# Performance work log

Measured on AMD Instinct MI355X. Metric: run time of the kernel, lower is better.

The kernel has to match this reference:

```python
import jax, jax.numpy as jnp
import numpy as np
from jax.scipy.special import logsumexp

B, N, K = 4, 2048, 20          # batch, points per cloud, knn neighbors
D_EMB, H = 512, 4              # embedding dim, attention heads
DH = D_EMB // H                # per-head dim (128)


def setup_inputs() -> dict:
    key = jax.random.key(0)
    ks = jax.random.split(key, 24)
    rn = lambda i, shape, s=0.05: jax.random.normal(ks[i], shape, jnp.float32) * s
    sc = lambda i, c: 1.0 + 0.1 * jax.random.normal(ks[i], (c,), jnp.float32)  # folded BN scale
    return {
        "src": jax.random.normal(ks[0], (B, 3, N), jnp.float32),
        "tgt": jax.random.normal(ks[1], (B, 3, N), jnp.float32),
        # GACLayer (shared for src/tgt): conv(6->64), conv(64->128), out conv(192->512); BN folded to scale/bias
        "g_w1": rn(2, (64, 6)),   "g_s1": sc(3, 64),  "g_b1": rn(4, (64,), 0.02),
        "g_w2": rn(5, (128, 64)), "g_s2": sc(6, 128), "g_b2": rn(7, (128,), 0.02),
        "g_wo": rn(8, (D_EMB, 192)), "g_so": sc(9, D_EMB), "g_bo": rn(10, (D_EMB,), 0.02),
        # MultiHeadedAttention: 3 projection 1x1 convs + merge (all with bias), mlp 1024->512 no bias
        "q_w": rn(11, (D_EMB, D_EMB)), "q_b": rn(12, (D_EMB,), 0.02),
        "k_w": rn(13, (D_EMB, D_EMB)), "k_b": rn(14, (D_EMB,), 0.02),
        "v_w": rn(15, (D_EMB, D_EMB)), "v_b": rn(16, (D_EMB,), 0.02),
        "m_w": rn(17, (D_EMB, D_EMB)), "m_b": rn(18, (D_EMB,), 0.02),
        "mlp_w": rn(19, (D_EMB, 2 * D_EMB)),
    }


def _forward(src, tgt, g_w1, g_s1, g_b1, g_w2, g_s2, g_b2, g_wo, g_so, g_bo,
             q_w, q_b, k_w, k_b, v_w, v_b, m_w, m_b, mlp_w):
    def knn_idx(x):                     # x: [B,3,N] -> [B,N,K] nearest-neighbor indices
        xx = jnp.sum(x * x, axis=1)                      # [B,N]
        inner = jnp.einsum('bdn,bdm->bnm', x, x)
        neg_d = 2.0 * inner - xx[:, :, None] - xx[:, None, :]   # negative sq dist
        return jax.lax.top_k(neg_d, K)[1]                # same as sort-descending[:k]

    def graph_feature(x):               # x: [B,D,N] -> [B,2D,N,K]
        idx = knn_idx(x)
        xt = x.transpose(0, 2, 1)                        # [B,N,D]
        feat = xt[jnp.arange(B)[:, None, None], idx]     # gather: [B,N,K,D]
        ctr = jnp.broadcast_to(xt[:, :, None, :], feat.shape)
        g = jnp.concatenate([feat - ctr, ctr], axis=-1)  # [B,N,K,2D]
        return g.transpose(0, 3, 1, 2)

    def conv_bn_relu2d(w, s, b, x):     # 1x1 conv2d + folded BN (eval) + relu
        y = jnp.einsum('oc,bcnk->bonk', w, x)
        return jax.nn.relu(y * s[:, None, None] + b[:, None, None])

    def attn_pool(h):                   # softmax over neighbors, weighted sum
        a = jax.nn.softmax(h, axis=-1)
        return jnp.sum(h * a, axis=-1)

    def gac(x):                         # GACLayer: [B,3,N] -> [B,512,N]
        g = graph_feature(x)            # [B,6,N,K]
        h1 = conv_bn_relu2d(g_w1, g_s1, g_b1, g)
        x1 = attn_pool(h1)              # [B,64,N]
        h2 = conv_bn_relu2d(g_w2, g_s2, g_b2, h1)
        x2 = attn_pool(h2)              # [B,128,N]
        o = jnp.einsum('oc,bcn->bon', g_wo, jnp.concatenate([x1, x2], axis=1))
        return jax.nn.relu(o * g_so[:, None] + g_bo[:, None])

    def proj(w, b, x):                  # 1x1 conv1d with bias
        return jnp.einsum('oi,bin->bon', w, x) + b[:, None]

    def mha(x, source):                 # note torch view splits channels as (dim, heads)
        q = proj(q_w, q_b, x).reshape(B, DH, H, -1)
        k_ = proj(k_w, k_b, source).reshape(B, DH, H, -1)
        v_ = proj(v_w, v_b, source).reshape(B, DH, H, -1)
        scores = jnp.einsum('bdhn,bdhm->bhnm', q, k_) / jnp.sqrt(jnp.float32(DH))
        prob = jax.nn.softmax(scores, axis=-1)
        msg = jnp.einsum('bhnm,bdhm->bdhn', prob, v_)
        return proj(m_w, m_b, msg.reshape(B, D_EMB, -1))

    def prop(x, source):                # AttentionalPropagation (mlp: 1024->512, no bias/relu)
        msg = mha(x, source)
        return jnp.einsum('oi,bin->bon', mlp_w, jnp.concatenate([x, msg], axis=1))

    def sinkhorn(scores, n_iters=5):    # log-domain Sinkhorn with dustbin row/col (zero pad)
        s = jnp.pad(scores, ((0, 0), (0, 1), (0, 1)))
        for _ in range(n_iters):
            s = jnp.concatenate(
                [s[:, :-1, :] - logsumexp(s[:, :-1, :], axis=2, keepdims=True), s[:, -1:, :]], axis=1)
            s = jnp.concatenate(
                [s[:, :, :-1] - logsumexp(s[:, :, :-1], axis=1, keepdims=True), s[:, :, -1:]], axis=2)
        return s[:, :-1, :-1]

    # embed + cross attentional GNN (shared layer, residual)
    d0, d1 = gac(src), gac(tgt)
    d0, d1 = d0 + prop(d0, d1), d1 + prop(d1, d0)

    dists = jnp.einsum('bdn,bdm->bnm', d0, d1) / jnp.sqrt(jnp.float32(D_EMB))
    perm = jnp.exp(sinkhorn(dists))
    perm_norm = perm / (jnp.sum(perm, axis=2, keepdims=True) + 1e-8)

    weighted_tgt = jnp.einsum('bdm,bnm->bdn', tgt, perm_norm)        # [B,3,N]
    weights = jnp.max(perm, axis=-1, keepdims=True)                  # [B,N,1]
    w_norm = (weights / (jnp.sum(weights, axis=1, keepdims=True) + 1e-8)).transpose(0, 2, 1)  # [B,1,N]
    src_c = jnp.sum(src * w_norm, axis=2, keepdims=True)             # [B,3,1]
    tgt_c = jnp.sum(weighted_tgt * w_norm, axis=2, keepdims=True)
    src_cent = src - src_c
    corr_cent = (weighted_tgt - tgt_c) * w_norm
    Hm = jnp.einsum('bdn,ben->bde', src_cent, corr_cent)             # [B,3,3]

    def solve(Hi):                      # Kabsch with reflection fix (torch.svd returns V, not V^T)
        u, s_, vt = jnp.linalg.svd(Hi)
        v = vt.T
        det = jnp.linalg.det(v @ u.T)
        diag = jnp.diag(jnp.concatenate([jnp.ones(2, Hi.dtype), det[None]]))
        return v @ diag @ u.T

    R = jax.vmap(solve)(Hm)
    t = (-jnp.einsum('bij,bjk->bik', R, src_c) + tgt_c).reshape(B, 3)
    return R, t, perm_norm


def reference(src, tgt, g_w1, g_s1, g_b1, g_w2, g_s2, g_b2, g_wo, g_so, g_bo,
              q_w, q_b, k_w, k_b, v_w, v_b, m_w, m_b, mlp_w):
    return _forward(src, tgt, g_w1, g_s1, g_b1, g_w2, g_s2, g_b2, g_wo, g_so, g_bo,
                    q_w, q_b, k_w, k_b, v_w, v_b, m_w, m_b, mlp_w)
```

## Files before the change

kernel.cpp:

```cpp
#include <hip/hip_runtime.h>
#include <math.h>

#define BATCH 4
#define NP    2048
#define KNNK  20
#define DEMB  512
#define NH    4
#define DHD   128

typedef __attribute__((ext_vector_type(8))) short bf16x8;
typedef __attribute__((ext_vector_type(4))) float f32x4;

__device__ __forceinline__ unsigned short f2b(float f) {
  unsigned u = __builtin_bit_cast(unsigned, f);
  u += 0x7FFF + ((u >> 16) & 1);
  return (unsigned short)(u >> 16);
}
__device__ __forceinline__ float b2f(unsigned short u) {
  unsigned v = ((unsigned)u) << 16;
  return __builtin_bit_cast(float, v);
}

__device__ __forceinline__ void gload_lds16(const void* g, void* l) {
  __builtin_amdgcn_global_load_lds(
      (const __attribute__((address_space(1))) unsigned int*)g,
      (__attribute__((address_space(3))) unsigned int*)l, 16, 0, 0);
}

__global__ void conv_all_kernel(const float* __restrict__ s0, const float* __restrict__ s1,
                                const float* __restrict__ s2, const float* __restrict__ s3,
                                const float* __restrict__ s4, const float* __restrict__ s5,
                                const float* __restrict__ s6,
                                unsigned short* __restrict__ d0, unsigned short* __restrict__ d1,
                                unsigned short* __restrict__ d2, unsigned short* __restrict__ d3,
                                unsigned short* __restrict__ d4, unsigned short* __restrict__ d5,
                                unsigned short* __restrict__ d6, float* __restrict__ vpot) {
  int i4 = (blockIdx.x * 256 + threadIdx.x) * 4;
  const float* src; unsigned short* dst; int off;
  if      (i4 < 262144)  { src = s0; dst = d0; off = i4; }
  else if (i4 < 524288)  { src = s1; dst = d1; off = i4 - 262144; }
  else if (i4 < 786432)  { src = s2; dst = d2; off = i4 - 524288; }
  else if (i4 < 1048576) { src = s3; dst = d3; off = i4 - 786432; }
  else if (i4 < 1572864) { src = s4; dst = d4; off = i4 - 1048576; }
  else if (i4 < 1581056) { src = s5; dst = d5; off = i4 - 1572864; }
  else if (i4 < 1679360) { src = s6; dst = d6; off = i4 - 1581056; }
  else if (i4 < 1687552) {
    off = i4 - 1679360;
    *(float4*)(vpot + off) = (float4){0.f, 0.f, 0.f, 0.f};
    return;
  } else return;
  float4 v = *(const float4*)(src + off);
  dst[off] = f2b(v.x); dst[off + 1] = f2b(v.y); dst[off + 2] = f2b(v.z); dst[off + 3] = f2b(v.w);
}

__global__ __launch_bounds__(256) void knn2_kernel(const float* __restrict__ x0,
                                                   const float* __restrict__ x1,
                                                   int* __restrict__ io0, int* __restrict__ io1) {
  __shared__ float xs0[NP], xs1[NP], xs2[NP];
  int which = blockIdx.x >> 11;
  int inner = blockIdx.x & 2047;
  const float* x = which ? x1 : x0;
  int* idx_out = which ? io1 : io0;
  int b = inner >> 9;
  int p0 = (inner & 511) * 4;
  int t = threadIdx.x, w = t >> 6, lane = t & 63;
  const float* xb = x + (size_t)b * 3 * NP;
  for (int m = t; m < NP; m += 256) {
    xs0[m] = xb[m]; xs1[m] = xb[NP + m]; xs2[m] = xb[2 * NP + m];
  }
  __syncthreads();
  int n = p0 + w;
  float c0 = xs0[n], c1 = xs1[n], c2 = xs2[n];
  float xxn = c0 * c0 + c1 * c1 + c2 * c2;
  float nd[32];
#pragma unroll
  for (int i = 0; i < 32; ++i) {
    int m = i * 64 + lane;
    float a0 = xs0[m], a1 = xs1[m], a2 = xs2[m];
    nd[i] = 2.f * (c0 * a0 + c1 * a1 + c2 * a2) - xxn - (a0 * a0 + a1 * a1 + a2 * a2);
  }
  unsigned sel = 0u;
  int* orow = idx_out + ((size_t)b * NP + n) * KNNK;
  for (int it = 0; it < KNNK; ++it) {
    float bv = -INFINITY; int bi = 0x7fffffff;
#pragma unroll
    for (int i = 0; i < 32; ++i) {
      float v = ((sel >> i) & 1u) ? -INFINITY : nd[i];
      if (v > bv) { bv = v; bi = i * 64 + lane; }
    }
#pragma unroll
    for (int s = 1; s < 64; s <<= 1) {
      float ov = __shfl_xor(bv, s);
      int oi = __shfl_xor(bi, s);
      if (ov > bv || (ov == bv && oi < bi)) { bv = ov; bi = oi; }
    }
    if (lane == 0) orow[it] = bi;
    if (lane == (bi & 63)) sel |= (1u << (bi >> 6));
  }
}

__global__ __launch_bounds__(256) void gac4_kernel(
    const float* __restrict__ x0, const float* __restrict__ x1,
    const int* __restrict__ io0, const int* __restrict__ io1,
    const float* __restrict__ w1, const float* __restrict__ s1, const float* __restrict__ b1,
    const unsigned short* __restrict__ w2b, const float* __restrict__ s2,
    const float* __restrict__ b2, unsigned short* __restrict__ xcg_all) {
  __shared__ __align__(16) float w1p[448];
  __shared__ float s1s[64], b1s[64];
  __shared__ float g[4][6][20];
  __shared__ __align__(16) float h1f[4][20][65];
  __shared__ __align__(16) unsigned short h1b[4 * 2048];
  int which = blockIdx.x >> 11;
  int inner = blockIdx.x & 2047;
  const float* x = which ? x1 : x0;
  const int* idx = which ? io1 : io0;
  unsigned short* xcg = xcg_all + (size_t)which * BATCH * NP * 192;
  int t = threadIdx.x, w = t >> 6, lane = t & 63;
  int lr = lane & 15, lg = lane >> 4;
  int b = inner >> 9;
  int n0g = (inner & 511) * 4;
  int pbase = b * NP + n0g;
  const float* xb = x + (size_t)b * 3 * NP;

  for (int i = t; i < 384; i += 256) { int o = i / 6, c = i % 6; w1p[o * 7 + c] = w1[i]; }
  if (t < 64) { s1s[t] = s1[t]; b1s[t] = b1[t]; }
  if (t < 80) {
    int p = t / 20, k = t % 20;
    int n = n0g + p;
    int j = idx[((size_t)b * NP + n) * KNNK + k];
    float c0 = xb[n], c1 = xb[NP + n], c2 = xb[2 * NP + n];
    g[p][0][k] = xb[j] - c0; g[p][1][k] = xb[NP + j] - c1; g[p][2][k] = xb[2 * NP + j] - c2;
    g[p][3][k] = c0; g[p][4][k] = c1; g[p][5][k] = c2;
  }
  for (int i = t; i < 4 * 12 * 32; i += 256) {
    int p = i / 384, rem = i % 384;
    ((unsigned*)h1b)[p * 1024 + (20 + rem / 32) * 32 + (rem & 31)] = 0u;
  }
  __syncthreads();

#pragma unroll
  for (int pass = 0; pass < 20; ++pass) {
    int item = pass * 256 + t;
    int o = item & 63, kp = item >> 6;
    int k = kp % 20, p = kp / 20;
    float y = 0.f;
#pragma unroll
    for (int c = 0; c < 6; ++c) y += w1p[o * 7 + c] * g[p][c][k];
    y = fmaxf(y * s1s[o] + b1s[o], 0.f);
    h1f[p][k][o] = y;
    h1b[p * 2048 + k * 64 + (((o >> 3) ^ (k & 7)) << 3) + (o & 7)] = f2b(y);
  }
  __syncthreads();

  {
    int p = w, o = lane;
    float mx = -INFINITY;
#pragma unroll
    for (int k = 0; k < 20; ++k) mx = fmaxf(mx, h1f[p][k][o]);
    float se = 0.f, sh = 0.f;
#pragma unroll
    for (int k = 0; k < 20; ++k) {
      float h = h1f[p][k][o];
      float e = __expf(h - mx);
      se += e; sh += h * e;
    }
    xcg[(size_t)(pbase + p) * 192 + o] = f2b(sh / se);
  }

  bf16x8 bfrag[2][2];
#pragma unroll
  for (int ks = 0; ks < 2; ++ks)
#pragma unroll
    for (int nt = 0; nt < 2; ++nt) {
      int kcol = nt * 16 + lr;
      int oc = ks * 4 + lg;
      bfrag[ks][nt] = *(const bf16x8*)&h1b[w * 2048 + kcol * 64 + ((oc ^ (kcol & 7)) << 3)];
    }
  f32x4 acc[8][2];
#pragma unroll
  for (int i = 0; i < 8; ++i) { acc[i][0] = (f32x4){0,0,0,0}; acc[i][1] = (f32x4){0,0,0,0}; }
#pragma unroll
  for (int i = 0; i < 8; ++i)
#pragma unroll
    for (int ks = 0; ks < 2; ++ks) {
      bf16x8 a = *(const bf16x8*)(w2b + (i * 16 + lr) * 64 + ks * 32 + lg * 8);
      acc[i][0] = __builtin_amdgcn_mfma_f32_16x16x32_bf16(a, bfrag[ks][0], acc[i][0], 0, 0, 0);
      acc[i][1] = __builtin_amdgcn_mfma_f32_16x16x32_bf16(a, bfrag[ks][1], acc[i][1], 0, 0, 0);
    }
  int pt = pbase + w;
#pragma unroll
  for (int i = 0; i < 8; ++i) {
    float x2o[4];
#pragma unroll
    for (int r = 0; r < 4; ++r) {
      int o = i * 16 + lg * 4 + r;
      float sv = s2[o], bv = b2[o];
      float v0 = fmaxf(acc[i][0][r] * sv + bv, 0.f);
      float v1 = fmaxf(acc[i][1][r] * sv + bv, 0.f);
      float vm = (lr < 4) ? fmaxf(v0, v1) : v0;
#pragma unroll
      for (int s = 1; s < 16; s <<= 1) vm = fmaxf(vm, __shfl_xor(vm, s));
      float e0 = __expf(v0 - vm);
      float e1 = (lr < 4) ? __expf(v1 - vm) : 0.f;
      float se = e0 + e1, sh = v0 * e0 + v1 * e1;
#pragma unroll
      for (int s = 1; s < 16; s <<= 1) { se += __shfl_xor(se, s); sh += __shfl_xor(sh, s); }
      x2o[r] = sh / se;
    }
    if (lr == 0) {
      ushort4 pk;
      pk.x = f2b(x2o[0]); pk.y = f2b(x2o[1]); pk.z = f2b(x2o[2]); pk.w = f2b(x2o[3]);
      *(ushort4*)&xcg[(size_t)pt * 192 + 64 + i * 16 + lg * 4] = pk;
    }
  }
}

__global__ __launch_bounds__(256, 2) void gacproj_kernel(
    const unsigned short* __restrict__ wob, const float* __restrict__ so,
    const float* __restrict__ bo, const unsigned short* __restrict__ xcg,
    unsigned short* __restrict__ Y0, unsigned short* __restrict__ Y1) {
  __shared__ __align__(16) unsigned short Al[128 * 64];
  __shared__ __align__(16) unsigned short Bl[128 * 64];
  int n0 = blockIdx.x * 128, o0 = blockIdx.y * 128;
  unsigned short* Yt = (n0 < BATCH * NP) ? Y0 : Y1;
  int nbase = n0 & (BATCH * NP - 1);
  int tid = threadIdx.x, w = tid >> 6, lane = tid & 63;
  int lr = lane & 15, lg = lane >> 4;
  int wa = w >> 1, wb = w & 1;
  f32x4 acc[4][4];
#pragma unroll
  for (int i = 0; i < 4; ++i)
#pragma unroll
    for (int j = 0; j < 4; ++j) acc[i][j] = (f32x4){0.f, 0.f, 0.f, 0.f};

  for (int k0 = 0; k0 < 192; k0 += 64) {
    __syncthreads();
#pragma unroll
    for (int u = 0; u < 4; ++u) {
      int C = u * 256 + tid;
      int row = C >> 3, j = C & 7;
      int js = j ^ (row & 7);
      gload_lds16(wob + (size_t)(o0 + row) * 192 + k0 + js * 8, Al + (u * 256 + w * 64) * 8);
      gload_lds16(xcg + (size_t)(n0 + row) * 192 + k0 + js * 8, Bl + (u * 256 + w * 64) * 8);
    }
    asm volatile("s_waitcnt vmcnt(0)" ::: "memory");
    __syncthreads();
#pragma unroll
    for (int kk = 0; kk < 2; ++kk) {
      bf16x8 af[4], bfr[4];
#pragma unroll
      for (int i = 0; i < 4; ++i) {
        int rowa = wa * 64 + i * 16 + lr;
        int ca = (kk * 4 + lg) ^ (rowa & 7);
        af[i] = *(const bf16x8*)(Al + rowa * 64 + ca * 8);
        int rowb = wb * 64 + i * 16 + lr;
        int cb = (kk * 4 + lg) ^ (rowb & 7);
        bfr[i] = *(const bf16x8*)(Bl + rowb * 64 + cb * 8);
      }
#pragma unroll
      for (int i = 0; i < 4; ++i)
#pragma unroll
        for (int j = 0; j < 4; ++j)
          acc[i][j] = __builtin_amdgcn_mfma_f32_16x16x32_bf16(af[i], bfr[j], acc[i][j], 0, 0, 0);
    }
  }
#pragma unroll
  for (int i = 0; i < 4; ++i) {
#pragma unroll
    for (int j = 0; j < 4; ++j) {
      int obase = o0 + wa * 64 + i * 16 + lg * 4;
      int n = nbase + wb * 64 + j * 16 + lr;
      ushort4 pk;
      pk.x = f2b(fmaxf(acc[i][j][0] * so[obase] + bo[obase], 0.f));
      pk.y = f2b(fmaxf(acc[i][j][1] * so[obase + 1] + bo[obase + 1], 0.f));
      pk.z = f2b(fmaxf(acc[i][j][2] * so[obase + 2] + bo[obase + 2], 0.f));
      pk.w = f2b(fmaxf(acc[i][j][3] * so[obase + 3] + bo[obase + 3], 0.f));
      *(ushort4*)&Yt[(size_t)n * DEMB + obase] = pk;
    }
  }
}

__global__ __launch_bounds__(256, 2) void qkv_kernel(
    const unsigned short* __restrict__ qw, const unsigned short* __restrict__ kw,
    const unsigned short* __restrict__ vw, const float* __restrict__ qbias,
    const float* __restrict__ kbias, const float* __restrict__ vbias,
    const unsigned short* __restrict__ d0t, const unsigned short* __restrict__ d1t,
    unsigned short* __restrict__ Q0, unsigned short* __restrict__ K0,
    unsigned short* __restrict__ V0, unsigned short* __restrict__ Q1,
    unsigned short* __restrict__ K1, unsigned short* __restrict__ V1) {
  __shared__ __align__(16) unsigned short Al[128 * 64];
  __shared__ __align__(16) unsigned short Bl[128 * 64];
  int z = blockIdx.z;
  int b = z & 3, which = z >> 2;
  int proj = which % 3, side = which / 3;
  const unsigned short* Wb = (proj == 0) ? qw : (proj == 1) ? kw : vw;
  const float* bias = (proj == 0) ? qbias : (proj == 1) ? kbias : vbias;
  const unsigned short* Bt = side ? d1t : d0t;
  unsigned short* Y = (which == 0) ? Q0 : (which == 1) ? K0 : (which == 2) ? V0
                    : (which == 3) ? Q1 : (which == 4) ? K1 : V1;
  float pscale = (proj == 0) ? 0.08838834764831845f : 1.f;
  int n0 = blockIdx.x * 128, o0 = blockIdx.y * 128;
  int tid = threadIdx.x, w = tid >> 6, lane = tid & 63;
  int lr = lane & 15, lg = lane >> 4;
  int wa = w >> 1, wb = w & 1;
  f32x4 acc[4][4];
#pragma unroll
  for (int i = 0; i < 4; ++i)
#pragma unroll
    for (int j = 0; j < 4; ++j) acc[i][j] = (f32x4){0.f, 0.f, 0.f, 0.f};

  for (int k0 = 0; k0 < DEMB; k0 += 64) {
    __syncthreads();
#pragma unroll
    for (int u = 0; u < 4; ++u) {
      int C = u * 256 + tid;
      int row = C >> 3, j = C & 7;
      int js = j ^ (row & 7);
      gload_lds16(Wb + (size_t)(o0 + row) * DEMB + k0 + js * 8, Al + (u * 256 + w * 64) * 8);
      gload_lds16(Bt + ((size_t)b * NP + n0 + row) * 512 + k0 + js * 8,
                  Bl + (u * 256 + w * 64) * 8);
    }
    asm volatile("s_waitcnt vmcnt(0)" ::: "memory");
    __syncthreads();
#pragma unroll
    for (int kk = 0; kk < 2; ++kk) {
      bf16x8 af[4], bfr[4];
#pragma unroll
      for (int i = 0; i < 4; ++i) {
        int rowa = wa * 64 + i * 16 + lr;
        int ca = (kk * 4 + lg) ^ (rowa & 7);
        af[i] = *(const bf16x8*)(Al + rowa * 64 + ca * 8);
        int rowb = wb * 64 + i * 16 + lr;
        int cb = (kk * 4 + lg) ^ (rowb & 7);
        bfr[i] = *(const bf16x8*)(Bl + rowb * 64 + cb * 8);
      }
#pragma unroll
      for (int i = 0; i < 4; ++i)
#pragma unroll
        for (int j = 0; j < 4; ++j)
          acc[i][j] = __builtin_amdgcn_mfma_f32_16x16x32_bf16(af[i], bfr[j], acc[i][j], 0, 0, 0);
    }
  }
#pragma unroll
  for (int i = 0; i < 4; ++i) {
#pragma unroll
    for (int j = 0; j < 4; ++j) {
#pragma unroll
      for (int r = 0; r < 4; ++r) {
        int o = o0 + wa * 64 + i * 16 + lg * 4 + r;
        int n = n0 + wb * 64 + j * 16 + lr;
        float v = (acc[i][j][r] + bias[o]) * pscale;
        int h = o & 3, dh = o >> 2;
        if (proj < 2) {
          Y[(((size_t)b * NH + h) * NP + n) * DHD + dh] = f2b(v);
        } else {
          Y[(((size_t)b * NH + h) * DHD + dh) * NP + n] = f2b(v);
        }
      }
    }
  }
}

template <int MODE, int KD>
__global__ __launch_bounds__(256, 2) void proj_mfma_kernel(
    const unsigned short* __restrict__ Wb, const float* __restrict__ bias,
    const unsigned short* __restrict__ Bt0, const unsigned short* __restrict__ Bt1,
    const unsigned short* __restrict__ Bt2_0, const unsigned short* __restrict__ Bt2_1,
    const unsigned short* __restrict__ D0, const unsigned short* __restrict__ D1,
    unsigned short* __restrict__ Y0, unsigned short* __restrict__ Y1) {
  __shared__ __align__(16) unsigned short Al[128 * 64];
  __shared__ __align__(16) unsigned short Bl[128 * 64];
  int z = blockIdx.z;
  int b = z & 3, side = z >> 2;
  const unsigned short* Bt = side ? Bt1 : Bt0;
  const unsigned short* Bt2 = side ? Bt2_1 : Bt2_0;
  const unsigned short* Dres = side ? D1 : D0;
  unsigned short* Y = side ? Y1 : Y0;
  int n0 = blockIdx.x * 128, o0 = blockIdx.y * 128;
  int tid = threadIdx.x, w = tid >> 6, lane = tid & 63;
  int lr = lane & 15, lg = lane >> 4;
  int wa = w >> 1, wb = w & 1;
  f32x4 acc[4][4];
#pragma unroll
  for (int i = 0; i < 4; ++i)
#pragma unroll
    for (int j = 0; j < 4; ++j) acc[i][j] = (f32x4){0.f, 0.f, 0.f, 0.f};

  for (int k0 = 0; k0 < KD; k0 += 64) {
    __syncthreads();
    const unsigned short* srcB; int kc;
    if (MODE == 4) { srcB = (k0 < 512) ? Bt : Bt2; kc = k0 & 511; }
    else { srcB = Bt; kc = k0; }
#pragma unroll
    for (int u = 0; u < 4; ++u) {
      int C = u * 256 + tid;
      int row = C >> 3, j = C & 7;
      int js = j ^ (row & 7);
      gload_lds16(Wb + (size_t)(o0 + row) * KD + k0 + js * 8, Al + (u * 256 + w * 64) * 8);
      gload_lds16(srcB + ((size_t)b * NP + n0 + row) * 512 + kc + js * 8,
                  Bl + (u * 256 + w * 64) * 8);
    }
    asm volatile("s_waitcnt vmcnt(0)" ::: "memory");
    __syncthreads();
#pragma unroll
    for (int kk = 0; kk < 2; ++kk) {
      bf16x8 af[4], bfr[4];
#pragma unroll
      for (int i = 0; i < 4; ++i) {
        int rowa = wa * 64 + i * 16 + lr;
        int ca = (kk * 4 + lg) ^ (rowa & 7);
        af[i] = *(const bf16x8*)(Al + rowa * 64 + ca * 8);
        int rowb = wb * 64 + i * 16 + lr;
        int cb = (kk * 4 + lg) ^ (rowb & 7);
        bfr[i] = *(const bf16x8*)(Bl + rowb * 64 + cb * 8);
      }
#pragma unroll
      for (int i = 0; i < 4; ++i)
#pragma unroll
        for (int j = 0; j < 4; ++j)
          acc[i][j] = __builtin_amdgcn_mfma_f32_16x16x32_bf16(af[i], bfr[j], acc[i][j], 0, 0, 0);
    }
  }
#pragma unroll
  for (int i = 0; i < 4; ++i) {
#pragma unroll
    for (int j = 0; j < 4; ++j) {
#pragma unroll
      for (int r = 0; r < 4; ++r) {
        int o = o0 + wa * 64 + i * 16 + lg * 4 + r;
        int n = n0 + wb * 64 + j * 16 + lr;
        float v = acc[i][j][r];
        if (MODE == 3) {
          v += bias[o];
        } else {
          v += b2f(Dres[((size_t)b * NP + n) * DEMB + o]);
        }
        Y[((size_t)b * NP + n) * DEMB + o] = f2b(v);
      }
    }
  }
}

__global__ __launch_bounds__(256, 2) void attn_mfma_kernel(
    const unsigned short* __restrict__ Q0, const unsigned short* __restrict__ K0,
    const unsigned short* __restrict__ V0, const unsigned short* __restrict__ Q1,
    const unsigned short* __restrict__ K1, const unsigned short* __restrict__ V1,
    unsigned short* __restrict__ att0, unsigned short* __restrict__ att1) {
  __shared__ __align__(16) unsigned short Klds[2][8192];
  __shared__ __align__(16) unsigned short Vlds[2][8192];
  __shared__ __align__(16) float Pws[4][544];

  int which = blockIdx.x >> 9;
  int blk = blockIdx.x & 511;
  const unsigned short* Qb = which ? Q1 : Q0;
  const unsigned short* Kb = which ? K0 : K1;
  const unsigned short* Vb = which ? V0 : V1;
  unsigned short* att = which ? att1 : att0;

  int bh = blk >> 5, qt = blk & 31;
  int tid = threadIdx.x;
  int w = tid >> 6, lane = tid & 63;
  int lr = lane & 15, lg = lane >> 4;
  int q0 = qt * 64 + w * 16;

  const unsigned short* Qrow = Qb + ((size_t)bh * NP + q0 + lr) * DHD + lg * 8;
  bf16x8 qf[4];
#pragma unroll
  for (int ds = 0; ds < 4; ++ds) qf[ds] = *(const bf16x8*)(Qrow + ds * 32);

  const unsigned short* Kg = Kb + (size_t)bh * NP * DHD;
  const unsigned short* Vg = Vb + (size_t)bh * DHD * NP;
  unsigned short* Pl = (unsigned short*)&Pws[w][0];

  f32x4 o[8];
#pragma unroll
  for (int ds = 0; ds < 8; ++ds) o[ds] = (f32x4){0.f, 0.f, 0.f, 0.f};
  float mrun[4] = {-INFINITY, -INFINITY, -INFINITY, -INFINITY};
  float lrun[4] = {0.f, 0.f, 0.f, 0.f};

#pragma unroll
  for (int u = 0; u < 4; ++u) {
    int C = (w * 4 + u) * 64 + lane;
    int key = C >> 4, jl = C & 15, j = jl ^ (key & 15);
    gload_lds16(Kg + (size_t)key * DHD + j * 8, &Klds[0][(w * 4 + u) * 512]);
    int d = C >> 3, jv = (C & 7) ^ (d & 7);
    gload_lds16(Vg + (size_t)d * NP + jv * 8, &Vlds[0][(w * 4 + u) * 512]);
  }
  asm volatile("s_waitcnt vmcnt(0)" ::: "memory");
  __syncthreads();

  for (int tIdx = 0; tIdx < 32; ++tIdx) {
    int cur = tIdx & 1;
    if (tIdx < 31) {
      int kv0 = (tIdx + 1) * 64;
#pragma unroll
      for (int u = 0; u < 4; ++u) {
        int C = (w * 4 + u) * 64 + lane;
        int key = C >> 4, jl = C & 15, j = jl ^ (key & 15);
        gload_lds16(Kg + (size_t)(kv0 + key) * DHD + j * 8, &Klds[cur ^ 1][(w * 4 + u) * 512]);
        int d = C >> 3, jv = (C & 7) ^ (d & 7);
        gload_lds16(Vg + (size_t)d * NP + kv0 + jv * 8, &Vlds[cur ^ 1][(w * 4 + u) * 512]);
      }
    }
    f32x4 s[4];
#pragma unroll
    for (int ks = 0; ks < 4; ++ks) {
      s[ks] = (f32x4){0.f, 0.f, 0.f, 0.f};
      int key = ks * 16 + lr;
#pragma unroll
      for (int dstep = 0; dstep < 4; ++dstep) {
        int dbyte = (lg * 16 + dstep * 64) ^ ((key & 15) << 4);
        bf16x8 kb = *(const bf16x8*)(&Klds[cur][0] + key * 128 + (dbyte >> 1));
        s[ks] = __builtin_amdgcn_mfma_f32_16x16x32_bf16(qf[dstep], kb, s[ks], 0, 0, 0);
      }
    }
    float tmax[4];
#pragma unroll
    for (int r = 0; r < 4; ++r) {
      float m = fmaxf(fmaxf(s[0][r], s[1][r]), fmaxf(s[2][r], s[3][r]));
#pragma unroll
      for (int msk = 1; msk < 16; msk <<= 1) m = fmaxf(m, __shfl_xor(m, msk));
      tmax[r] = m;
    }
    int need = 0;
#pragma unroll
    for (int r = 0; r < 4; ++r) need |= (tmax[r] > mrun[r]) ? 1 : 0;
    float fac[4] = {1.f, 1.f, 1.f, 1.f};
    if (__any(need)) {
#pragma unroll
      for (int r = 0; r < 4; ++r) {
        float mnew = fmaxf(mrun[r], tmax[r]);
        fac[r] = __expf(mrun[r] - mnew);
        mrun[r] = mnew;
      }
#pragma unroll
      for (int ds = 0; ds < 8; ++ds)
#pragma unroll
        for (int r = 0; r < 4; ++r) o[ds][r] *= fac[r];
    }
    float ps[4] = {0.f, 0.f, 0.f, 0.f};
#pragma unroll
    for (int ks = 0; ks < 4; ++ks) {
      int k = ks * 16 + lr;
#pragma unroll
      for (int r = 0; r < 4; ++r) {
        float p = __expf(s[ks][r] - mrun[r]);
        ps[r] += p;
        int q = lg * 4 + r;
        int kbyte = (k * 2) ^ ((q & 7) << 4);
        Pl[q * 64 + (kbyte >> 1)] = f2b(p);
      }
    }
#pragma unroll
    for (int r = 0; r < 4; ++r) {
#pragma unroll
      for (int msk = 1; msk < 16; msk <<= 1) ps[r] += __shfl_xor(ps[r], msk);
      lrun[r] = lrun[r] * fac[r] + ps[r];
    }
#pragma unroll
    for (int ks2 = 0; ks2 < 2; ++ks2) {
      int kbyte = ((lg * 8 + ks2 * 32) * 2) ^ ((lr & 7) << 4);
      bf16x8 pa = *(const bf16x8*)(Pl + lr * 64 + (kbyte >> 1));
#pragma unroll
      for (int ds = 0; ds < 8; ++ds) {
        int d = ds * 16 + lr;
        int keybyte = ((lg * 8 + ks2 * 32) * 2) ^ ((d & 7) << 4);
        bf16x8 vb = *(const bf16x8*)(&Vlds[cur][0] + d * 64 + (keybyte >> 1));
        o[ds] = __builtin_amdgcn_mfma_f32_16x16x32_bf16(pa, vb, o[ds], 0, 0, 0);
      }
    }
    asm volatile("s_waitcnt vmcnt(0)" ::: "memory");
    __syncthreads();
  }

  float linv[4];
#pragma unroll
  for (int r = 0; r < 4; ++r) linv[r] = 1.f / lrun[r];
  float* ost = &Pws[w][0];
  int b = bh >> 2, h = bh & 3;
  unsigned short* outb = att + ((size_t)b * NP + q0) * DEMB;
#pragma unroll
  for (int c = 0; c < 4; ++c) {
#pragma unroll
    for (int half = 0; half < 2; ++half) {
      int ds = 2 * c + half;
#pragma unroll
      for (int r = 0; r < 4; ++r)
        ost[(lg * 4 + r) * 33 + half * 16 + lr] = o[ds][r] * linv[r];
    }
    __syncthreads();
#pragma unroll
    for (int it = 0; it < 8; ++it) {
      int q = lr, dl = it * 4 + lg;
      int d = c * 32 + dl;
      outb[(size_t)q * DEMB + d * 4 + h] = f2b(ost[q * 33 + dl]);
    }
    __syncthreads();
  }
}

__global__ __launch_bounds__(256, 2) void dists_mfma_kernel(
    const unsigned short* __restrict__ At, const unsigned short* __restrict__ Bt,
    unsigned short* __restrict__ S) {
  __shared__ __align__(16) unsigned short Sh[2][8192];
  int b = blockIdx.z;
  int n0 = blockIdx.y * 128, m0 = blockIdx.x * 128;
  int tid = threadIdx.x, w = tid >> 6, lane = tid & 63;
  int lr = lane & 15, lg = lane >> 4;
  int wn = w >> 1, wm = w & 1;
  const unsigned short* Ab = At + ((size_t)b * NP + n0) * DEMB;
  const unsigned short* Bb = Bt + ((size_t)b * NP + m0) * DEMB;
  f32x4 acc[4][4];
#pragma unroll
  for (int i = 0; i < 4; ++i)
#pragma unroll
    for (int j = 0; j < 4; ++j) acc[i][j] = (f32x4){0.f, 0.f, 0.f, 0.f};

  for (int k0 = 0; k0 < DEMB; k0 += 64) {
    __syncthreads();
#pragma unroll
    for (int u = 0; u < 4; ++u) {
      int C = u * 256 + tid;
      int row = C >> 3, j = C & 7;
      int js = j ^ (row & 7);
      gload_lds16(Ab + (size_t)row * DEMB + k0 + js * 8, &Sh[0][(u * 256 + w * 64) * 8]);
      gload_lds16(Bb + (size_t)row * DEMB + k0 + js * 8, &Sh[1][(u * 256 + w * 64) * 8]);
    }
    asm volatile("s_waitcnt vmcnt(0)" ::: "memory");
    __syncthreads();
#pragma unroll
    for (int kk = 0; kk < 2; ++kk) {
      bf16x8 af[4], bfr[4];
#pragma unroll
      for (int i = 0; i < 4; ++i) {
        int rowa = wn * 64 + i * 16 + lr;
        int ca = (kk * 4 + lg) ^ (rowa & 7);
        af[i] = *(const bf16x8*)(&Sh[0][0] + rowa * 64 + ca * 8);
        int rowb = wm * 64 + i * 16 + lr;
        int cb = (kk * 4 + lg) ^ (rowb & 7);
        bfr[i] = *(const bf16x8*)(&Sh[1][0] + rowb * 64 + cb * 8);
      }
#pragma unroll
      for (int i = 0; i < 4; ++i)
#pragma unroll
        for (int j = 0; j < 4; ++j)
          acc[i][j] = __builtin_amdgcn_mfma_f32_16x16x32_bf16(af[i], bfr[j], acc[i][j], 0, 0, 0);
    }
  }
  const float scale = 0.04419417382415922f;
  __syncthreads();
  unsigned short* Cs = &Sh[0][0];
#pragma unroll
  for (int i = 0; i < 4; ++i)
#pragma unroll
    for (int j = 0; j < 4; ++j)
#pragma unroll
      for (int r = 0; r < 4; ++r) {
        int nl = wn * 64 + i * 16 + lg * 4 + r;
        int ml = wm * 64 + j * 16 + lr;
        Cs[nl * 128 + ml] = f2b(acc[i][j][r] * scale);
      }
  __syncthreads();
  unsigned short* Sb = S + (size_t)b * NP * NP;
#pragma unroll
  for (int it = 0; it < 8; ++it) {
    int chunk = it * 256 + tid;
    int rowl = chunk >> 4, c8 = (chunk & 15) * 8;
    *(bf16x8*)(Sb + (size_t)(n0 + rowl) * NP + m0 + c8) = *(const bf16x8*)(Cs + rowl * 128 + c8);
  }
}

__global__ __launch_bounds__(256) void sink_u_kernel(const unsigned short* __restrict__ S,
                                                     const float* __restrict__ v,
                                                     float* __restrict__ u) {
  int t = threadIdx.x, w = t >> 6, lane = t & 63;
  int rowid = blockIdx.x * 4 + w;
  int b = rowid >> 11, i = rowid & 2047;
  const unsigned short* row = S + ((size_t)b * NP + i) * NP;
  const float* vb = v + (size_t)b * NP;
  float m = -INFINITY, s = 0.f;
#pragma unroll
  for (int c = 0; c < 4; ++c) {
    int off = c * 512 + lane * 8;
    bf16x8 x8 = *(const bf16x8*)(row + off);
    float4 va = *(const float4*)(vb + off);
    float4 vc = *(const float4*)(vb + off + 4);
    float xs[8];
    xs[0] = b2f(x8[0]) + va.x; xs[1] = b2f(x8[1]) + va.y;
    xs[2] = b2f(x8[2]) + va.z; xs[3] = b2f(x8[3]) + va.w;
    xs[4] = b2f(x8[4]) + vc.x; xs[5] = b2f(x8[5]) + vc.y;
    xs[6] = b2f(x8[6]) + vc.z; xs[7] = b2f(x8[7]) + vc.w;
    float mc = fmaxf(fmaxf(fmaxf(xs[0], xs[1]), fmaxf(xs[2], xs[3])),
                     fmaxf(fmaxf(xs[4], xs[5]), fmaxf(xs[6], xs[7])));
    float sc = 0.f;
#pragma unroll
    for (int e = 0; e < 8; ++e) sc += __expf(xs[e] - mc);
    float M = fmaxf(m, mc);
    s = s * __expf(m - M) + sc * __expf(mc - M);
    m = M;
  }
#pragma unroll
  for (int st = 1; st < 64; st <<= 1) {
    float m2 = __shfl_xor(m, st), s2 = __shfl_xor(s, st);
    float M = fmaxf(m, m2);
    s = s * __expf(m - M) + s2 * __expf(m2 - M);
    m = M;
  }
  if (lane == 0) {
    float M = fmaxf(m, 0.f);
    float ss = s * __expf(m - M) + __expf(-M);
    u[(size_t)b * NP + i] = -(M + logf(ss));
  }
}

__global__ void sink_c1_kernel(const unsigned short* __restrict__ S, const float* __restrict__ u,
                               float* __restrict__ colM, float* __restrict__ colS) {
  int ctile = blockIdx.x, part = blockIdx.y, b = blockIdx.z;
  int t = threadIdx.x, ry = t >> 6, cx = t & 63;
  int c0 = ctile * 128 + cx * 2;
  int rbase = part * 256 + ry * 64;
  const unsigned short* Sb = S + (size_t)b * NP * NP;
  const float* ub = u + (size_t)b * NP;
  float m0 = -INFINITY, s0 = 0.f, m1 = -INFINITY, s1 = 0.f;
  for (int r8 = 0; r8 < 64; r8 += 8) {
    float x0[8], x1[8];
#pragma unroll
    for (int k = 0; k < 8; ++k) {
      int r = rbase + r8 + k;
      unsigned pk = *(const unsigned*)(Sb + (size_t)r * NP + c0);
      float uu = ub[r];
      x0[k] = b2f((unsigned short)pk) + uu;
      x1[k] = b2f((unsigned short)(pk >> 16)) + uu;
    }
    float mc0 = x0[0], mc1 = x1[0];
#pragma unroll
    for (int k = 1; k < 8; ++k) { mc0 = fmaxf(mc0, x0[k]); mc1 = fmaxf(mc1, x1[k]); }
    float sc0 = 0.f, sc1 = 0.f;
#pragma unroll
    for (int k = 0; k < 8; ++k) { sc0 += __expf(x0[k] - mc0); sc1 += __expf(x1[k] - mc1); }
    float M0 = fmaxf(m0, mc0);
    s0 = s0 * __expf(m0 - M0) + sc0 * __expf(mc0 - M0); m0 = M0;
    float M1 = fmaxf(m1, mc1);
    s1 = s1 * __expf(m1 - M1) + sc1 * __expf(mc1 - M1); m1 = M1;
  }
  __shared__ float pm[4][128], ps[4][128];
  pm[ry][cx * 2] = m0; pm[ry][cx * 2 + 1] = m1;
  ps[ry][cx * 2] = s0; ps[ry][cx * 2 + 1] = s1;
  __syncthreads();
  if (t < 128) {
    float m = pm[0][t], s = ps[0][t];
    for (int k = 1; k < 4; ++k) {
      float m2 = pm[k][t], s2 = ps[k][t];
      float M = fmaxf(m, m2);
      s = s * __expf(m - M) + s2 * __expf(m2 - M);
      m = M;
    }
    size_t oo = ((size_t)b * NP + ctile * 128 + t) * 8 + part;
    colM[oo] = m; colS[oo] = s;
  }
}

__global__ void sink_c2_kernel(const float* __restrict__ colM, const float* __restrict__ colS,
                               float* __restrict__ v) {
  int i = blockIdx.x * 256 + threadIdx.x;
  if (i >= BATCH * NP) return;
  float m = -INFINITY, s = 0.f;
  for (int p = 0; p < 8; ++p) {
    float m2 = colM[(size_t)i * 8 + p], s2 = colS[(size_t)i * 8 + p];
    float M = fmaxf(m, m2);
    s = s * __expf(m - M) + s2 * __expf(m2 - M);
    m = M;
  }
  float M = fmaxf(m, 0.f);
  s = s * __expf(m - M) + __expf(-M);
  v[i] = -(M + logf(s));
}

__global__ void perm_kernel(const unsigned short* __restrict__ S, const float* __restrict__ u,
                            const float* __restrict__ v, const float* __restrict__ tgt,
                            float* __restrict__ outp, float* __restrict__ weights,
                            float* __restrict__ wt) {
  int b = blockIdx.x / NP, n = blockIdx.x % NP, t = threadIdx.x;
  const unsigned short* row = S + ((size_t)b * NP + n) * NP;
  const float* vb = v + (size_t)b * NP;
  float ui = u[(size_t)b * NP + n];
  __shared__ float reds[256], redm[256];
  int c0 = t * 8;
  bf16x8 x8 = *(const bf16x8*)(row + c0);
  float4 va = *(const float4*)(vb + c0);
  float4 vc = *(const float4*)(vb + c0 + 4);
  float ev[8];
  ev[0] = __expf(b2f(x8[0]) + ui + va.x); ev[1] = __expf(b2f(x8[1]) + ui + va.y);
  ev[2] = __expf(b2f(x8[2]) + ui + va.z); ev[3] = __expf(b2f(x8[3]) + ui + va.w);
  ev[4] = __expf(b2f(x8[4]) + ui + vc.x); ev[5] = __expf(b2f(x8[5]) + ui + vc.y);
  ev[6] = __expf(b2f(x8[6]) + ui + vc.z); ev[7] = __expf(b2f(x8[7]) + ui + vc.w);
  float lsum = 0.f, lm = -INFINITY;
#pragma unroll
  for (int e = 0; e < 8; ++e) { lsum += ev[e]; lm = fmaxf(lm, ev[e]); }
  reds[t] = lsum; redm[t] = lm;
  __syncthreads();
  for (int st = 128; st > 0; st >>= 1) {
    if (t < st) { reds[t] += reds[t + st]; redm[t] = fmaxf(redm[t], redm[t + st]); }
    __syncthreads();
  }
  float inv = 1.f / (reds[0] + 1e-8f);
  float mx = redm[0];
  __syncthreads();
  const float* tb = tgt + (size_t)b * 3 * NP;
  float* op = outp + ((size_t)b * NP + n) * NP;
  float pn[8];
#pragma unroll
  for (int e = 0; e < 8; ++e) pn[e] = ev[e] * inv;
  float4 o0 = {pn[0], pn[1], pn[2], pn[3]};
  float4 o1 = {pn[4], pn[5], pn[6], pn[7]};
  *(float4*)(op + c0) = o0;
  *(float4*)(op + c0 + 4) = o1;
  float av[3];
#pragma unroll
  for (int d = 0; d < 3; ++d) {
    const float* td = tb + d * NP;
    float4 ta = *(const float4*)(td + c0);
    float4 tc = *(const float4*)(td + c0 + 4);
    av[d] = pn[0] * ta.x + pn[1] * ta.y + pn[2] * ta.z + pn[3] * ta.w +
            pn[4] * tc.x + pn[5] * tc.y + pn[6] * tc.z + pn[7] * tc.w;
  }
  for (int d = 0; d < 3; ++d) {
    reds[t] = av[d];
    __syncthreads();
    for (int st = 128; st > 0; st >>= 1) { if (t < st) reds[t] += reds[t + st]; __syncthreads(); }
    if (t == 0) wt[((size_t)b * 3 + d) * NP + n] = reds[0];
    __syncthreads();
  }
  if (t == 0) weights[(size_t)b * NP + n] = mx;
}

__global__ void wsum_kernel(const float* __restrict__ weights, float* __restrict__ wsum) {
  int b = blockIdx.x, t = threadIdx.x;
  __shared__ float red[256];
  float s = 0.f;
  for (int n = t; n < NP; n += 256) s += weights[(size_t)b * NP + n];
  red[t] = s;
  __syncthreads();
  for (int st = 128; st > 0; st >>= 1) { if (t < st) red[t] += red[t + st]; __syncthreads(); }
  if (t == 0) wsum[b] = red[0];
}

__global__ void cent_hm_kernel(const float* __restrict__ src, const float* __restrict__ wt,
                               const float* __restrict__ weights, const float* __restrict__ wsum,
                               float* __restrict__ cent, float* __restrict__ Hm) {
  int b = blockIdx.x, t = threadIdx.x;
  __shared__ float red[256];
  __shared__ float cc[6];
  float inv = 1.f / (wsum[b] + 1e-8f);
  const float* sb = src + (size_t)b * 3 * NP;
  const float* wb = wt + (size_t)b * 3 * NP;
  const float* ww = weights + (size_t)b * NP;
  float acc[6] = {};
  for (int n = t; n < NP; n += 256) {
    float w = ww[n] * inv;
    acc[0] += sb[n] * w;        acc[1] += sb[NP + n] * w;  acc[2] += sb[2 * NP + n] * w;
    acc[3] += wb[n] * w;        acc[4] += wb[NP + n] * w;  acc[5] += wb[2 * NP + n] * w;
  }
  for (int i = 0; i < 6; ++i) {
    red[t] = acc[i];
    __syncthreads();
    for (int st = 128; st > 0; st >>= 1) { if (t < st) red[t] += red[t + st]; __syncthreads(); }
    if (t == 0) cc[i] = red[0];
    __syncthreads();
  }
  float h[9] = {};
  for (int n = t; n < NP; n += 256) {
    float w = ww[n] * inv;
    float s0 = sb[n] - cc[0], s1 = sb[NP + n] - cc[1], s2 = sb[2 * NP + n] - cc[2];
    float d0 = (wb[n] - cc[3]) * w, d1 = (wb[NP + n] - cc[4]) * w, d2 = (wb[2 * NP + n] - cc[5]) * w;
    h[0] += s0 * d0; h[1] += s0 * d1; h[2] += s0 * d2;
    h[3] += s1 * d0; h[4] += s1 * d1; h[5] += s1 * d2;
    h[6] += s2 * d0; h[7] += s2 * d1; h[8] += s2 * d2;
  }
  for (int i = 0; i < 9; ++i) {
    red[t] = h[i];
    __syncthreads();
    for (int st = 128; st > 0; st >>= 1) { if (t < st) red[t] += red[t + st]; __syncthreads(); }
    if (t == 0) Hm[b * 9 + i] = red[0];
    __syncthreads();
  }
  if (t == 0) for (int i = 0; i < 6; ++i) cent[b * 6 + i] = cc[i];
}

__device__ double det3d(const double M[3][3]) {
  return M[0][0] * (M[1][1] * M[2][2] - M[1][2] * M[2][1])
       - M[0][1] * (M[1][0] * M[2][2] - M[1][2] * M[2][0])
       + M[0][2] * (M[1][0] * M[2][1] - M[1][1] * M[2][0]);
}

#define JROT(p, q)                                                              \
  do {                                                                          \
    double apq = S[p][q];                                                       \
    if (fabs(apq) > 1e-60) {                                                    \
      double tau = (S[q][q] - S[p][p]) / (2.0 * apq);                           \
      double tt = (tau >= 0.0) ? 1.0 / (tau + sqrt(1.0 + tau * tau))            \
                               : 1.0 / (tau - sqrt(1.0 + tau * tau));           \
      double cr = 1.0 / sqrt(1.0 + tt * tt), sr = tt * cr;                      \
      _Pragma("unroll") for (int k = 0; k < 3; ++k) {                           \
        double skp = S[k][p], skq = S[k][q];                                    \
        S[k][p] = cr * skp - sr * skq;  S[k][q] = sr * skp + cr * skq;          \
      }                                                                         \
      _Pragma("unroll") for (int k = 0; k < 3; ++k) {                           \
        double spk = S[p][k], sqk = S[q][k];                                    \
        S[p][k] = cr * spk - sr * sqk;  S[q][k] = sr * spk + cr * sqk;          \
      }                                                                         \
      _Pragma("unroll") for (int k = 0; k < 3; ++k) {                           \
        double vkp = V[k][p], vkq = V[k][q];                                    \
        V[k][p] = cr * vkp - sr * vkq;  V[k][q] = sr * vkp + cr * vkq;          \
      }                                                                         \
    }                                                                           \
  } while (0)

#define CSWAPCOL(i, j, ei, ej)                                                  \
  if (ei < ej) {                                                                \
    double tt_ = ei; ei = ej; ej = tt_;                                         \
    _Pragma("unroll") for (int r = 0; r < 3; ++r) {                             \
      double tv = V[r][i]; V[r][i] = V[r][j]; V[r][j] = tv;                     \
    }                                                                           \
  }

__global__ void solve_kernel(const float* __restrict__ Hm, const float* __restrict__ cent,
                             float* __restrict__ out) {
  int b = threadIdx.x;
  if (b >= BATCH) return;
  double A[3][3];
#pragma unroll
  for (int r = 0; r < 3; ++r)
#pragma unroll
    for (int c = 0; c < 3; ++c) A[r][c] = (double)Hm[b * 9 + r * 3 + c];
  double S[3][3];
#pragma unroll
  for (int i = 0; i < 3; ++i)
#pragma unroll
    for (int j = 0; j < 3; ++j) {
      double acc = 0.0;
#pragma unroll
      for (int k = 0; k < 3; ++k) acc += A[k][i] * A[k][j];
      S[i][j] = acc;
    }
  double V[3][3] = {{1, 0, 0}, {0, 1, 0}, {0, 0, 1}};
  for (int sweep = 0; sweep < 12; ++sweep) {
    JROT(0, 1); JROT(0, 2); JROT(1, 2);
  }
  double e0 = S[0][0], e1 = S[1][1], e2 = S[2][2];
  CSWAPCOL(0, 1, e0, e1);
  CSWAPCOL(0, 2, e0, e2);
  CSWAPCOL(1, 2, e1, e2);
  double Us[3][3];
#pragma unroll
  for (int i = 0; i < 3; ++i) {
    double v0 = V[0][i], v1 = V[1][i], v2 = V[2][i];
    double u0 = A[0][0] * v0 + A[0][1] * v1 + A[0][2] * v2;
    double u1 = A[1][0] * v0 + A[1][1] * v1 + A[1][2] * v2;
    double u2 = A[2][0] * v0 + A[2][1] * v1 + A[2][2] * v2;
    double nrm = sqrt(u0 * u0 + u1 * u1 + u2 * u2);
    if (nrm > 1e-30) { u0 /= nrm; u1 /= nrm; u2 /= nrm; }
    else if (i == 2) {
      u0 = Us[1][0] * Us[2][1] - Us[2][0] * Us[1][1];
      u1 = Us[2][0] * Us[0][1] - Us[0][0] * Us[2][1];
      u2 = Us[0][0] * Us[1][1] - Us[1][0] * Us[0][1];
      double nn = sqrt(u0 * u0 + u1 * u1 + u2 * u2);
      if (nn > 1e-30) { u0 /= nn; u1 /= nn; u2 /= nn; }
    }
    Us[0][i] = u0; Us[1][i] = u1; Us[2][i] = u2;
  }
  double d = det3d(V) * det3d(Us);
  double R[3][3];
#pragma unroll
  for (int i = 0; i < 3; ++i)
#pragma unroll
    for (int j = 0; j < 3; ++j)
      R[i][j] = V[i][0] * Us[j][0] + V[i][1] * Us[j][1] + d * V[i][2] * Us[j][2];
  double sc[3] = {(double)cent[b * 6 + 0], (double)cent[b * 6 + 1], (double)cent[b * 6 + 2]};
  double tc[3] = {(double)cent[b * 6 + 3], (double)cent[b * 6 + 4], (double)cent[b * 6 + 5]};
#pragma unroll
  for (int r = 0; r < 3; ++r)
#pragma unroll
    for (int c = 0; c < 3; ++c) out[b * 9 + r * 3 + c] = (float)R[r][c];
#pragma unroll
  for (int i = 0; i < 3; ++i) {
    double tv = tc[i] - (R[i][0] * sc[0] + R[i][1] * sc[1] + R[i][2] * sc[2]);
    out[36 + b * 3 + i] = (float)tv;
  }
}

extern "C" void kernel_launch(void* const* d_in, const int* in_sizes, int n_in,
                              void* d_out, int out_size, void* d_ws, size_t ws_size,
                              hipStream_t stream) {
  const float* src  = (const float*)d_in[0];
  const float* tgt  = (const float*)d_in[1];
  const float* g_w1 = (const float*)d_in[2];
  const float* g_s1 = (const float*)d_in[3];
  const float* g_b1 = (const float*)d_in[4];
  const float* g_w2 = (const float*)d_in[5];
  const float* g_s2 = (const float*)d_in[6];
  const float* g_b2 = (const float*)d_in[7];
  const float* g_wo = (const float*)d_in[8];
  const float* g_so = (const float*)d_in[9];
  const float* g_bo = (const float*)d_in[10];
  const float* q_w  = (const float*)d_in[11];
  const float* q_b  = (const float*)d_in[12];
  const float* k_w  = (const float*)d_in[13];
  const float* k_b  = (const float*)d_in[14];
  const float* v_w  = (const float*)d_in[15];
  const float* v_b  = (const float*)d_in[16];
  const float* m_w  = (const float*)d_in[17];
  const float* m_b  = (const float*)d_in[18];
  const float* mlp_w = (const float*)d_in[19];
  float* out = (float*)d_out;
  float* ws = (float*)d_ws;

  const size_t SLOT = 4194304;
  unsigned short* d0t  = (unsigned short*)(ws + 0 * SLOT);
  unsigned short* d1t  = (unsigned short*)(ws + 1 * SLOT);
  unsigned short* Q0   = (unsigned short*)(ws + 2 * SLOT);
  unsigned short* K0   = (unsigned short*)(ws + 3 * SLOT);
  unsigned short* V0   = (unsigned short*)(ws + 4 * SLOT);
  unsigned short* Q1   = (unsigned short*)(ws + 5 * SLOT);
  unsigned short* K1   = (unsigned short*)(ws + 6 * SLOT);
  unsigned short* V1   = (unsigned short*)(ws + 7 * SLOT);
  unsigned short* att0t = (unsigned short*)(ws + 8 * SLOT);
  unsigned short* att1t = (unsigned short*)(ws + 9 * SLOT);
  unsigned short* mp0t = Q0;
  unsigned short* mp1t = Q1;
  unsigned short* d0nt = att0t;
  unsigned short* d1nt = att1t;
  unsigned short* base3  = (unsigned short*)(ws + 3 * SLOT);
  unsigned short* q_wb   = base3 + 4456448;
  unsigned short* k_wb   = q_wb + 262144;
  unsigned short* v_wb   = k_wb + 262144;
  unsigned short* m_wb   = v_wb + 262144;
  unsigned short* mlp_wb = m_wb + 262144;
  unsigned short* w2b    = mlp_wb + 524288;
  unsigned short* wob    = w2b + 8192;
  unsigned short* xcg    = att0t;
  unsigned short* SbU = (unsigned short*)ws;
  int*   idx0 = (int*)(ws + 10 * SLOT);
  int*   idx1 = idx0 + BATCH * NP * KNNK;
  float* colM = ws + 10 * SLOT + 327680;
  float* colS = colM + BATCH * NP * 8;
  float* weights = colS + BATCH * NP * 8;
  float* wsum = weights + BATCH * NP;
  float* wtg  = wsum + BATCH;
  float* cent = wtg + BATCH * 3 * NP;
  float* Hmb  = cent + BATCH * 6;
  float* upot = Hmb + BATCH * 9;
  float* vpot = upot + BATCH * NP;

  conv_all_kernel<<<1648, 256, 0, stream>>>(q_w, k_w, v_w, m_w, mlp_w, g_w2, g_wo,
                                            q_wb, k_wb, v_wb, m_wb, mlp_wb, w2b, wob, vpot);
  knn2_kernel<<<2 * BATCH * NP / 4, 256, 0, stream>>>(src, tgt, idx0, idx1);
  gac4_kernel<<<2 * BATCH * NP / 4, 256, 0, stream>>>(src, tgt, idx0, idx1, g_w1, g_s1, g_b1,
                                                      w2b, g_s2, g_b2, xcg);
  dim3 gg(2 * BATCH * NP / 128, DEMB / 128);
  gacproj_kernel<<<gg, 256, 0, stream>>>(wob, g_so, g_bo, xcg, d0t, d1t);
  dim3 gqkv(NP / 128, DEMB / 128, 24);
  qkv_kernel<<<gqkv, 256, 0, stream>>>(q_wb, k_wb, v_wb, q_b, k_b, v_b, d0t, d1t,
                                       Q0, K0, V0, Q1, K1, V1);
  attn_mfma_kernel<<<2 * 16 * 32, 256, 0, stream>>>(Q0, K0, V0, Q1, K1, V1, att0t, att1t);
  dim3 gq8(NP / 128, DEMB / 128, 8);
  proj_mfma_kernel<3, 512><<<gq8, 256, 0, stream>>>(m_wb, m_b, att0t, att1t, nullptr, nullptr,
                                                    nullptr, nullptr, mp0t, mp1t);
  proj_mfma_kernel<4, 1024><<<gq8, 256, 0, stream>>>(mlp_wb, nullptr, d0t, d1t, mp0t, mp1t,
                                                     d0t, d1t, d0nt, d1nt);
  dists_mfma_kernel<<<dim3(NP / 128, NP / 128, BATCH), 256, 0, stream>>>(d0nt, d1nt, SbU);
  for (int it = 0; it < 5; ++it) {
    sink_u_kernel<<<BATCH * NP / 4, 256, 0, stream>>>(SbU, vpot, upot);
    sink_c1_kernel<<<dim3(NP / 128, 8, BATCH), 256, 0, stream>>>(SbU, upot, colM, colS);
    sink_c2_kernel<<<(BATCH * NP + 255) / 256, 256, 0, stream>>>(colM, colS, vpot);
  }
  perm_kernel<<<BATCH * NP, 256, 0, stream>>>(SbU, upot, vpot, tgt, out + 48, weights, wtg);
  wsum_kernel<<<BATCH, 256, 0, stream>>>(weights, wsum);
  cent_hm_kernel<<<BATCH, 256, 0, stream>>>(src, wtg, weights, wsum, cent, Hmb);
  solve_kernel<<<1, 64, 0, stream>>>(Hmb, cent, out);
}
```

Measured before the change: 680.9 us.

## Load V directly into registers in attention, drop V LDS staging, raise occupancy

The attention kernel stops staging V tiles through LDS and instead loads each wave's V fragments straight from global memory into registers at the start of every KV step. This frees half the LDS, which allows the launch bound to go from 2 to 3 blocks per CU. The change also raises wave priority around the MFMA sections and removes the block barriers in the per-wave output staging epilogue. The risks are that the V global loads are no longer prefetched a tile ahead, so their latency is exposed in each iteration, 16 extra vector registers per thread add pressure, and several waves now fetch the same V rows from global memory.

Measured after the change: 996.9 us. 1.46x slower.

```diff
diff --git a/kernel.cpp b/kernel.cpp
--- a/kernel.cpp
+++ b/kernel.cpp
@@ -441,13 +441,12 @@
   }
 }
 
-__global__ __launch_bounds__(256, 2) void attn_mfma_kernel(
+__global__ __launch_bounds__(256, 3) void attn_mfma_kernel(
     const unsigned short* __restrict__ Q0, const unsigned short* __restrict__ K0,
     const unsigned short* __restrict__ V0, const unsigned short* __restrict__ Q1,
     const unsigned short* __restrict__ K1, const unsigned short* __restrict__ V1,
     unsigned short* __restrict__ att0, unsigned short* __restrict__ att1) {
   __shared__ __align__(16) unsigned short Klds[2][8192];
-  __shared__ __align__(16) unsigned short Vlds[2][8192];
   __shared__ __align__(16) float Pws[4][544];
 
   int which = blockIdx.x >> 9;
@@ -483,25 +482,30 @@
     int C = (w * 4 + u) * 64 + lane;
     int key = C >> 4, jl = C & 15, j = jl ^ (key & 15);
     gload_lds16(Kg + (size_t)key * DHD + j * 8, &Klds[0][(w * 4 + u) * 512]);
-    int d = C >> 3, jv = (C & 7) ^ (d & 7);
-    gload_lds16(Vg + (size_t)d * NP + jv * 8, &Vlds[0][(w * 4 + u) * 512]);
   }
   asm volatile("s_waitcnt vmcnt(0)" ::: "memory");
   __syncthreads();
 
   for (int tIdx = 0; tIdx < 32; ++tIdx) {
     int cur = tIdx & 1;
+    int kv0 = tIdx * 64;
+    bf16x8 vreg[16];
+#pragma unroll
+    for (int ks2 = 0; ks2 < 2; ++ks2)
+#pragma unroll
+      for (int ds = 0; ds < 8; ++ds)
+        vreg[ks2 * 8 + ds] =
+            *(const bf16x8*)(Vg + (size_t)(ds * 16 + lr) * NP + kv0 + ks2 * 32 + lg * 8);
     if (tIdx < 31) {
-      int kv0 = (tIdx + 1) * 64;
+      int kn = kv0 + 64;
 #pragma unroll
       for (int u = 0; u < 4; ++u) {
         int C = (w * 4 + u) * 64 + lane;
         int key = C >> 4, jl = C & 15, j = jl ^ (key & 15);
-        gload_lds16(Kg + (size_t)(kv0 + key) * DHD + j * 8, &Klds[cur ^ 1][(w * 4 + u) * 512]);
-        int d = C >> 3, jv = (C & 7) ^ (d & 7);
-        gload_lds16(Vg + (size_t)d * NP + kv0 + jv * 8, &Vlds[cur ^ 1][(w * 4 + u) * 512]);
+        gload_lds16(Kg + (size_t)(kn + key) * DHD + j * 8, &Klds[cur ^ 1][(w * 4 + u) * 512]);
       }
     }
+    __builtin_amdgcn_s_setprio(1);
     f32x4 s[4];
 #pragma unroll
     for (int ks = 0; ks < 4; ++ks) {
@@ -514,6 +518,7 @@
         s[ks] = __builtin_amdgcn_mfma_f32_16x16x32_bf16(qf[dstep], kb, s[ks], 0, 0, 0);
       }
     }
+    __builtin_amdgcn_s_setprio(0);
     float tmax[4];
 #pragma unroll
     for (int r = 0; r < 4; ++r) {
@@ -557,18 +562,16 @@
       for (int msk = 1; msk < 16; msk <<= 1) ps[r] += __shfl_xor(ps[r], msk);
       lrun[r] = lrun[r] * fac[r] + ps[r];
     }
+    __builtin_amdgcn_s_setprio(1);
 #pragma unroll
     for (int ks2 = 0; ks2 < 2; ++ks2) {
       int kbyte = ((lg * 8 + ks2 * 32) * 2) ^ ((lr & 7) << 4);
       bf16x8 pa = *(const bf16x8*)(Pl + lr * 64 + (kbyte >> 1));
 #pragma unroll
-      for (int ds = 0; ds < 8; ++ds) {
-        int d = ds * 16 + lr;
-        int keybyte = ((lg * 8 + ks2 * 32) * 2) ^ ((d & 7) << 4);
-        bf16x8 vb = *(const bf16x8*)(&Vlds[cur][0] + d * 64 + (keybyte >> 1));
-        o[ds] = __builtin_amdgcn_mfma_f32_16x16x32_bf16(pa, vb, o[ds], 0, 0, 0);
-      }
-    }
+      for (int ds = 0; ds < 8; ++ds)
+        o[ds] = __builtin_amdgcn_mfma_f32_16x16x32_bf16(pa, vreg[ks2 * 8 + ds], o[ds], 0, 0, 0);
+    }
+    __builtin_amdgcn_s_setprio(0);
     asm volatile("s_waitcnt vmcnt(0)" ::: "memory");
     __syncthreads();
   }
@@ -588,14 +591,12 @@
       for (int r = 0; r < 4; ++r)
         ost[(lg * 4 + r) * 33 + half * 16 + lr] = o[ds][r] * linv[r];
     }
-    __syncthreads();
 #pragma unroll
     for (int it = 0; it < 8; ++it) {
       int q = lr, dl = it * 4 + lg;
       int d = c * 32 + dl;
       outb[(size_t)q * DEMB + d * 4 + h] = f2b(ost[q * 33 + dl]);
     }
-    __syncthreads();
   }
 }
 
```
